# Kernel tuning notes

Hardware: AMD Instinct MI355X
Metric: run time of the kernel (lower is better)

## Reference

```python
import jax, jax.numpy as jnp
import numpy as np

LAM_CONSIST = 0.1
LAM_LR = 1.0
LAM_PAIR = 1.0


def _cubic(x, a=-0.75):
    # PyTorch bicubic kernel (a = -0.75)
    ax = jnp.abs(x)
    ax2 = ax * ax
    ax3 = ax2 * ax
    f1 = (a + 2.0) * ax3 - (a + 3.0) * ax2 + 1.0
    f2 = a * ax3 - 5.0 * a * ax2 + 8.0 * a * ax - 4.0 * a
    return jnp.where(ax <= 1.0, f1, jnp.where(ax < 2.0, f2, 0.0))


def _resize_matrix(in_size: int, out_size: int) -> jnp.ndarray:
    """Weight matrix [out_size, in_size] for antialiased bicubic resize
    (align_corners=False, antialias=True, border replicate) as in
    F.interpolate(..., mode='bicubic', antialias=True)."""
    scale = in_size / out_size
    s_aa = max(scale, 1.0)  # widen kernel when downscaling (antialias)
    support = 2.0 * s_aa
    ext = int(np.ceil(support)) + 1
    centers = (np.arange(out_size, dtype=np.float64) + 0.5) * scale - 0.5
    idx = np.arange(-ext, in_size + ext)
    dist = (idx[None, :] - centers[:, None]) / s_aa  # [out, in+2ext]
    w = _cubic(jnp.asarray(dist, dtype=jnp.float32))
    w = w / jnp.sum(w, axis=1, keepdims=True)  # torch normalizes window weights
    idx_c = np.clip(idx, 0, in_size - 1)  # clamp -> replicate border
    M = jnp.zeros((out_size, in_size), dtype=jnp.float32).at[:, idx_c].add(w)
    return M


def _resize_bicubic_aa(img: jnp.ndarray, th: int, tw: int) -> jnp.ndarray:
    # img: [B, C, H, W] -> [B, C, th, tw], separable resize via two matmuls
    _, _, h, w = img.shape
    Mh = _resize_matrix(h, th)  # [th, h]
    Mw = _resize_matrix(w, tw)  # [tw, w]
    return jnp.einsum('oh,bchw,pw->bcop', Mh, img, Mw)


def setup_inputs() -> dict:
    key = jax.random.key(0)
    k1, k2, k3 = jax.random.split(key, 3)
    pred_hr = jax.random.normal(k1, (32, 3, 512, 512), dtype=jnp.float32)
    target_hr = jax.random.normal(k2, (32, 3, 512, 512), dtype=jnp.float32)
    lr_ref = jax.random.normal(k3, (32, 3, 128, 128), dtype=jnp.float32)
    scale = jnp.full((32,), 4.0, dtype=jnp.float32)  # uniform -> static sizes
    return {"pred_hr": pred_hr, "target_hr": target_hr, "lr_ref": lr_ref, "scale": scale}


def reference(pred_hr, target_hr, lr_ref, scale):
    pix = jnp.mean(jnp.abs(pred_hr - target_hr))
    # project_scale(pred_hr, src=scale, dst=1): uniform scale=4 ->
    # target size == lr_ref spatial size (static, read from lr_ref shape)
    th, tw = lr_ref.shape[-2], lr_ref.shape[-1]
    pred_lr = _resize_bicubic_aa(pred_hr, th, tw)
    lr_term = jnp.mean(jnp.abs(pred_lr - lr_ref))
    pair_term = jnp.float32(0.0)  # pair_pred_hr / pair_scale are None
    consist = LAM_LR * lr_term + LAM_PAIR * pair_term
    total = pix + LAM_CONSIST * consist
    return (total, pix, consist, lr_term, pair_term)
```

## Files before the change

kernel.cpp:

```cpp
#include <hip/hip_runtime.h>

#define HW    512
#define OUTW  128
#define NIMG  96
#define N_HR  ((long long)NIMG*HW*HW)
#define N_LR  ((long long)NIMG*OUTW*OUTW)
#define NPART (NIMG*64)

__device__ __forceinline__ float cubic075(float x){
    float ax = fabsf(x);
    float ax2 = ax*ax, ax3 = ax2*ax;
    const float A = -0.75f;
    float f1 = (A+2.f)*ax3 - (A+3.f)*ax2 + 1.f;
    float f2 = A*ax3 - 5.f*A*ax2 + 8.f*A*ax - 4.f*A;
    return ax <= 1.f ? f1 : (ax < 2.f ? f2 : 0.f);
}

__device__ __forceinline__ void get_weights(float w[16]){
    float s = 0.f;
#pragma unroll
    for (int k = 0; k < 16; ++k){
        float d = ((float)k - 7.5f) * 0.25f;
        w[k] = cubic075(d);
        s += w[k];
    }
#pragma unroll
    for (int k = 0; k < 16; ++k) w[k] /= s;
}

__global__ __launch_bounds__(256) void kmain(const float* __restrict__ pred,
                                             const float* __restrict__ tgt,
                                             const float* __restrict__ lr,
                                             double* __restrict__ part){
    const int img = blockIdx.x >> 4;
    const int tid = threadIdx.x;
    const int w   = tid >> 6;
    const int l   = tid & 63;
    const int gw  = ((blockIdx.x & 15) << 2) + w;
    const int o0  = gw << 1;
    const int s   = (gw << 3) - 6;

    float wt[16]; get_weights(wt);
    const float* P = pred + (size_t)img * (HW*HW);
    const float* T = tgt  + (size_t)img * (HW*HW);
    const float* L = lr   + (size_t)img * (OUTW*OUTW);

    float acc[2][2] = {{0.f,0.f},{0.f,0.f}};
    float pix_acc = 0.f, lr_acc = 0.f;

    int r0 = min(HW-1, max(0, s + 0));
    int r1 = min(HW-1, max(0, s + 1));
    const float4* rp0 = (const float4*)(P + (size_t)r0 * HW);
    const float4* rp1 = (const float4*)(P + (size_t)r1 * HW);
    float4 c0 = rp0[2*l], c1 = rp0[2*l+1];
    float4 n0 = rp1[2*l], n1 = rp1[2*l+1];
    float4 tc0, tc1, tn0, tn1;

#pragma unroll 4
    for (int i = 0; i < 20; ++i){
        float4 f0, f1, tf0, tf1;
        if (i < 18){
            int rn = min(HW-1, max(0, s + i + 2));
            const float4* rp = (const float4*)(P + (size_t)rn * HW);
            f0 = rp[2*l]; f1 = rp[2*l+1];
        }
        if (i + 2 >= 6 && i + 2 < 14){
            const float4* tp = (const float4*)(T + (size_t)(s + i + 2) * HW);
            tf0 = tp[2*l]; tf1 = tp[2*l+1];
        }

        const float p0=c0.x,p1v=c0.y,p2v=c0.z,p3=c0.w,
                    p4=c1.x,p5=c1.y,p6=c1.z,p7=c1.w;

        if (i >= 6 && i < 14){
            pix_acc += fabsf(p0-tc0.x)+fabsf(p1v-tc0.y)+fabsf(p2v-tc0.z)+fabsf(p3-tc0.w)
                     + fabsf(p4-tc1.x)+fabsf(p5-tc1.y)+fabsf(p6-tc1.z)+fabsf(p7-tc1.w);
        }

        float Lm6 = __shfl_up(p2v,1,64), Lm5 = __shfl_up(p3,1,64),
              Lm4 = __shfl_up(p4,1,64),  Lm3 = __shfl_up(p5,1,64),
              Lm2 = __shfl_up(p6,1,64),  Lm1 = __shfl_up(p7,1,64);
        float R8  = __shfl_down(p0,1,64), R9  = __shfl_down(p1v,1,64),
              R10 = __shfl_down(p2v,1,64),R11 = __shfl_down(p3,1,64),
              R12 = __shfl_down(p4,1,64), R13 = __shfl_down(p5,1,64);
        if (l == 0){ Lm6=p0; Lm5=p0; Lm4=p0; Lm3=p0; Lm2=p0; Lm1=p0; }
        if (l == 63){ R8=p7; R9=p7; R10=p7; R11=p7; R12=p7; R13=p7; }

        float w20[20] = {Lm6,Lm5,Lm4,Lm3,Lm2,Lm1,p0,p1v,p2v,p3,p4,p5,p6,p7,
                         R8,R9,R10,R11,R12,R13};
        float h0 = 0.f, h1 = 0.f;
#pragma unroll
        for (int k = 0; k < 16; ++k){
            h0 += wt[k]*w20[k];
            h1 += wt[k]*w20[k+4];
        }

#pragma unroll
        for (int q = 0; q < 2; ++q){
            int k = i - 4*q;
            if (k >= 0 && k < 16){
                acc[q][0] += wt[k]*h0;
                acc[q][1] += wt[k]*h1;
            }
        }

        c0=n0; c1=n1; n0=f0; n1=f1;
        tc0=tn0; tc1=tn1; tn0=tf0; tn1=tf1;
    }

#pragma unroll
    for (int q = 0; q < 2; ++q){
        const float2 lv = *(const float2*)(L + (size_t)(o0+q)*OUTW + 2*l);
        lr_acc += fabsf(acc[q][0]-lv.x) + fabsf(acc[q][1]-lv.y);
    }

#pragma unroll
    for (int off = 32; off > 0; off >>= 1){
        pix_acc += __shfl_down(pix_acc, off, 64);
        lr_acc  += __shfl_down(lr_acc,  off, 64);
    }
    if (l == 0){
        const int slot = (blockIdx.x << 2) + w;
        part[slot]         = (double)pix_acc;
        part[NPART + slot] = (double)lr_acc;
    }
}

__global__ __launch_bounds__(256) void k3(const double* __restrict__ part,
                                          float* __restrict__ out){
    const int t = threadIdx.x;
    double v1 = 0.0, v2 = 0.0;
    for (int i = t; i < NPART; i += 256){
        v1 += part[i];
        v2 += part[NPART + i];
    }
#pragma unroll
    for (int off = 32; off > 0; off >>= 1){
        v1 += __shfl_down(v1, off, 64);
        v2 += __shfl_down(v2, off, 64);
    }
    __shared__ double s1[4], s2[4];
    const int lane = t & 63, wid = t >> 6;
    if (lane == 0){ s1[wid] = v1; s2[wid] = v2; }
    __syncthreads();
    if (t == 0){
        double S1 = s1[0]+s1[1]+s1[2]+s1[3];
        double S2 = s2[0]+s2[1]+s2[2]+s2[3];
        float pix     = (float)(S1 / (double)N_HR);
        float lr_term = (float)(S2 / (double)N_LR);
        float pair    = 0.f;
        float consist = 1.0f * lr_term + 1.0f * pair;
        float total   = pix + 0.1f * consist;
        out[0] = total; out[1] = pix; out[2] = consist; out[3] = lr_term; out[4] = pair;
    }
}

extern "C" void kernel_launch(void* const* d_in, const int* in_sizes, int n_in,
                              void* d_out, int out_size, void* d_ws, size_t ws_size,
                              hipStream_t stream){
    const float* pred = (const float*)d_in[0];
    const float* tgt  = (const float*)d_in[1];
    const float* lrr  = (const float*)d_in[2];
    float* out = (float*)d_out;

    double* part = (double*)d_ws;

    kmain<<<NIMG*16, 256, 0, stream>>>(pred, tgt, lrr, part);
    k3<<<1, 256, 0, stream>>>(part, out);
}
```

Baseline: 236.5 us.

## Split fused resize into separate horizontal and vertical pass kernels via intermediate buffer

Replaces the single fused kernel, which streamed a sliding 20-row window per wave, with a row-parallel kernel that reads each pred/target row once, computes the L1 pixel term and the horizontal bicubic pass, and writes a horizontally-resized intermediate. A second kernel performs the vertical 16-tap pass from that buffer and computes the LR term. This removes the roughly 2.5x redundant row reads and the serial per-wave loop, exposing far more parallel waves, with blocks swizzled across XCDs. In exchange it adds an intermediate buffer write/read, an extra launch, and a larger partial-sum reduction in the final single-block kernel.

```diff
diff --git a/kernel.cpp b/kernel.cpp
--- a/kernel.cpp
+++ b/kernel.cpp
@@ -5,7 +5,10 @@
 #define NIMG  96
 #define N_HR  ((long long)NIMG*HW*HW)
 #define N_LR  ((long long)NIMG*OUTW*OUTW)
-#define NPART (NIMG*64)
+
+#define NPIXS (NIMG*HW/1)
+#define NLRS  (NIMG*OUTW)
+#define HSTR  (HW*OUTW)
 
 __device__ __forceinline__ float cubic075(float x){
     float ax = fabsf(x);
@@ -28,112 +31,96 @@
     for (int k = 0; k < 16; ++k) w[k] /= s;
 }
 
-__global__ __launch_bounds__(256) void kmain(const float* __restrict__ pred,
-                                             const float* __restrict__ tgt,
-                                             const float* __restrict__ lr,
-                                             double* __restrict__ part){
-    const int img = blockIdx.x >> 4;
-    const int tid = threadIdx.x;
-    const int w   = tid >> 6;
-    const int l   = tid & 63;
-    const int gw  = ((blockIdx.x & 15) << 2) + w;
-    const int o0  = gw << 1;
-    const int s   = (gw << 3) - 6;
+
+__global__ __launch_bounds__(256) void k1(const float* __restrict__ pred,
+                                          const float* __restrict__ tgt,
+                                          double* __restrict__ partPix,
+                                          float* __restrict__ hbuf){
+    const int b       = blockIdx.x;
+    const int logical = ((b & 7) * 1536) + (b >> 3);
+    const int w   = threadIdx.x >> 6;
+    const int l   = threadIdx.x & 63;
+    const int task = (logical << 2) + w;
+    const int img  = task >> 9;
+    const int row  = task & 511;
 
     float wt[16]; get_weights(wt);
-    const float* P = pred + (size_t)img * (HW*HW);
-    const float* T = tgt  + (size_t)img * (HW*HW);
-    const float* L = lr   + (size_t)img * (OUTW*OUTW);
+    const float4* Pr = (const float4*)(pred + (size_t)img*(HW*HW) + (size_t)row*HW);
+    const float4* Tr = (const float4*)(tgt  + (size_t)img*(HW*HW) + (size_t)row*HW);
 
-    float acc[2][2] = {{0.f,0.f},{0.f,0.f}};
-    float pix_acc = 0.f, lr_acc = 0.f;
+    const float4 c0 = Pr[2*l], c1 = Pr[2*l+1];
+    const float4 t0 = Tr[2*l], t1 = Tr[2*l+1];
+    const float p0=c0.x,p1v=c0.y,p2v=c0.z,p3=c0.w,
+                p4=c1.x,p5=c1.y,p6=c1.z,p7=c1.w;
 
-    int r0 = min(HW-1, max(0, s + 0));
-    int r1 = min(HW-1, max(0, s + 1));
-    const float4* rp0 = (const float4*)(P + (size_t)r0 * HW);
-    const float4* rp1 = (const float4*)(P + (size_t)r1 * HW);
-    float4 c0 = rp0[2*l], c1 = rp0[2*l+1];
-    float4 n0 = rp1[2*l], n1 = rp1[2*l+1];
-    float4 tc0, tc1, tn0, tn1;
+    float pix_acc = fabsf(p0-t0.x)+fabsf(p1v-t0.y)+fabsf(p2v-t0.z)+fabsf(p3-t0.w)
+                  + fabsf(p4-t1.x)+fabsf(p5-t1.y)+fabsf(p6-t1.z)+fabsf(p7-t1.w);
 
-#pragma unroll 4
-    for (int i = 0; i < 20; ++i){
-        float4 f0, f1, tf0, tf1;
-        if (i < 18){
-            int rn = min(HW-1, max(0, s + i + 2));
-            const float4* rp = (const float4*)(P + (size_t)rn * HW);
-            f0 = rp[2*l]; f1 = rp[2*l+1];
-        }
-        if (i + 2 >= 6 && i + 2 < 14){
-            const float4* tp = (const float4*)(T + (size_t)(s + i + 2) * HW);
-            tf0 = tp[2*l]; tf1 = tp[2*l+1];
-        }
+    float Lm6 = __shfl_up(p2v,1,64), Lm5 = __shfl_up(p3,1,64),
+          Lm4 = __shfl_up(p4,1,64),  Lm3 = __shfl_up(p5,1,64),
+          Lm2 = __shfl_up(p6,1,64),  Lm1 = __shfl_up(p7,1,64);
+    float R8  = __shfl_down(p0,1,64), R9  = __shfl_down(p1v,1,64),
+          R10 = __shfl_down(p2v,1,64),R11 = __shfl_down(p3,1,64),
+          R12 = __shfl_down(p4,1,64), R13 = __shfl_down(p5,1,64);
+    if (l == 0){ Lm6=p0; Lm5=p0; Lm4=p0; Lm3=p0; Lm2=p0; Lm1=p0; }
+    if (l == 63){ R8=p7; R9=p7; R10=p7; R11=p7; R12=p7; R13=p7; }
 
-        const float p0=c0.x,p1v=c0.y,p2v=c0.z,p3=c0.w,
-                    p4=c1.x,p5=c1.y,p6=c1.z,p7=c1.w;
+    float w20[20] = {Lm6,Lm5,Lm4,Lm3,Lm2,Lm1,p0,p1v,p2v,p3,p4,p5,p6,p7,
+                     R8,R9,R10,R11,R12,R13};
+    float h0 = 0.f, h1 = 0.f;
+#pragma unroll
+    for (int k = 0; k < 16; ++k){
+        h0 += wt[k]*w20[k];
+        h1 += wt[k]*w20[k+4];
+    }
 
-        if (i >= 6 && i < 14){
-            pix_acc += fabsf(p0-tc0.x)+fabsf(p1v-tc0.y)+fabsf(p2v-tc0.z)+fabsf(p3-tc0.w)
-                     + fabsf(p4-tc1.x)+fabsf(p5-tc1.y)+fabsf(p6-tc1.z)+fabsf(p7-tc1.w);
-        }
-
-        float Lm6 = __shfl_up(p2v,1,64), Lm5 = __shfl_up(p3,1,64),
-              Lm4 = __shfl_up(p4,1,64),  Lm3 = __shfl_up(p5,1,64),
-              Lm2 = __shfl_up(p6,1,64),  Lm1 = __shfl_up(p7,1,64);
-        float R8  = __shfl_down(p0,1,64), R9  = __shfl_down(p1v,1,64),
-              R10 = __shfl_down(p2v,1,64),R11 = __shfl_down(p3,1,64),
-              R12 = __shfl_down(p4,1,64), R13 = __shfl_down(p5,1,64);
-        if (l == 0){ Lm6=p0; Lm5=p0; Lm4=p0; Lm3=p0; Lm2=p0; Lm1=p0; }
-        if (l == 63){ R8=p7; R9=p7; R10=p7; R11=p7; R12=p7; R13=p7; }
-
-        float w20[20] = {Lm6,Lm5,Lm4,Lm3,Lm2,Lm1,p0,p1v,p2v,p3,p4,p5,p6,p7,
-                         R8,R9,R10,R11,R12,R13};
-        float h0 = 0.f, h1 = 0.f;
-#pragma unroll
-        for (int k = 0; k < 16; ++k){
-            h0 += wt[k]*w20[k];
-            h1 += wt[k]*w20[k+4];
-        }
+    ((float2*)(hbuf + (size_t)img*HSTR + (size_t)row*OUTW))[l] = make_float2(h0, h1);
 
 #pragma unroll
-        for (int q = 0; q < 2; ++q){
-            int k = i - 4*q;
-            if (k >= 0 && k < 16){
-                acc[q][0] += wt[k]*h0;
-                acc[q][1] += wt[k]*h1;
-            }
-        }
+    for (int off = 32; off > 0; off >>= 1)
+        pix_acc += __shfl_down(pix_acc, off, 64);
+    if (l == 0) partPix[task] = (double)pix_acc;
+}
 
-        c0=n0; c1=n1; n0=f0; n1=f1;
-        tc0=tn0; tc1=tn1; tn0=tf0; tn1=tf1;
+__global__ __launch_bounds__(256) void k2(const float* __restrict__ hbuf,
+                                          const float* __restrict__ lr,
+                                          double* __restrict__ partLr){
+    const int b       = blockIdx.x;
+    const int logical = ((b & 7) * 384) + (b >> 3);
+    const int w   = threadIdx.x >> 6;
+    const int l   = threadIdx.x & 63;
+    const int task = (logical << 2) + w;
+    const int img  = task >> 7;
+    const int o    = task & 127;
+
+    float wt[16]; get_weights(wt);
+    const float* base = hbuf + (size_t)img*HSTR;
+
+    float a0 = 0.f, a1 = 0.f;
+#pragma unroll
+    for (int k = 0; k < 16; ++k){
+        const int r = min(HW-1, max(0, 4*o - 6 + k));
+        const float2 hv = ((const float2*)(base + (size_t)r*OUTW))[l];
+        a0 += wt[k]*hv.x;
+        a1 += wt[k]*hv.y;
     }
 
-#pragma unroll
-    for (int q = 0; q < 2; ++q){
-        const float2 lv = *(const float2*)(L + (size_t)(o0+q)*OUTW + 2*l);
-        lr_acc += fabsf(acc[q][0]-lv.x) + fabsf(acc[q][1]-lv.y);
-    }
+    const float2 lv = ((const float2*)(lr + (size_t)img*(OUTW*OUTW) + (size_t)o*OUTW))[l];
+    float lr_acc = fabsf(a0-lv.x) + fabsf(a1-lv.y);
 
 #pragma unroll
-    for (int off = 32; off > 0; off >>= 1){
-        pix_acc += __shfl_down(pix_acc, off, 64);
-        lr_acc  += __shfl_down(lr_acc,  off, 64);
-    }
-    if (l == 0){
-        const int slot = (blockIdx.x << 2) + w;
-        part[slot]         = (double)pix_acc;
-        part[NPART + slot] = (double)lr_acc;
-    }
+    for (int off = 32; off > 0; off >>= 1)
+        lr_acc += __shfl_down(lr_acc, off, 64);
+    if (l == 0) partLr[task] = (double)lr_acc;
 }
 
-__global__ __launch_bounds__(256) void k3(const double* __restrict__ part,
+__global__ __launch_bounds__(256) void k3(const double* __restrict__ partPix,
+                                          const double* __restrict__ partLr,
                                           float* __restrict__ out){
     const int t = threadIdx.x;
     double v1 = 0.0, v2 = 0.0;
-    for (int i = t; i < NPART; i += 256){
-        v1 += part[i];
-        v2 += part[NPART + i];
-    }
+    for (int i = t; i < NPIXS; i += 256) v1 += partPix[i];
+    for (int i = t; i < NLRS;  i += 256) v2 += partLr[i];
 #pragma unroll
     for (int off = 32; off > 0; off >>= 1){
         v1 += __shfl_down(v1, off, 64);
@@ -163,8 +150,11 @@
     const float* lrr  = (const float*)d_in[2];
     float* out = (float*)d_out;
 
-    double* part = (double*)d_ws;
+    double* partPix = (double*)d_ws;
+    double* partLr  = partPix + NPIXS;
+    float*  hbuf    = (float*)(partLr + NLRS);
 
-    kmain<<<NIMG*16, 256, 0, stream>>>(pred, tgt, lrr, part);
-    k3<<<1, 256, 0, stream>>>(part, out);
+    k1<<<NIMG*HW/4, 256, 0, stream>>>(pred, tgt, partPix, hbuf);
+    k2<<<NIMG*OUTW/4, 256, 0, stream>>>(hbuf, lrr, partLr);
+    k3<<<1, 256, 0, stream>>>(partPix, partLr, out);
 }
```

Result: slower. 292.6 us (+23.7%).
